# Performance work log

Hardware: AMD Instinct MI355X
Metric: run time of the kernel (lower is better)

The kernel has to match this reference:

```python
import jax, jax.numpy as jnp
import numpy as np

B, C, H, W, L = 2, 64, 48, 48, 48
GH, GW, GL = 24, 24, 24  # gating signal at half resolution


def setup_inputs() -> dict:
    key = jax.random.key(0)
    k = jax.random.split(key, 6)
    x = jax.random.normal(k[0], (B, C, H, W, L), dtype=jnp.float32)
    g = jax.random.normal(k[1], (B, C, GH, GW, GL), dtype=jnp.float32)
    s = 1.0 / np.sqrt(C)
    W1 = jax.random.normal(k[2], (C, C), dtype=jnp.float32) * s  # conv1 1x1x1 weight (out,in)
    b1 = jax.random.normal(k[3], (C,), dtype=jnp.float32) * 0.01
    W2 = jax.random.normal(k[4], (C, C), dtype=jnp.float32) * s  # conv2 1x1x1 weight
    b2 = jax.random.normal(k[5], (C,), dtype=jnp.float32) * 0.01
    return {"x": x, "g": g, "W1": W1, "b1": b1, "W2": W2, "b2": b2}


def _conv1x1(v, Wm, b):
    # 1x1x1 Conv3d == channel-mixing matmul
    return jnp.einsum('bchwl,oc->bohwl', v, Wm) + b[None, :, None, None, None]


def reference(x, g, W1, b1, W2, b2):
    theta_x = _conv1x1(x, W1, b1)                       # (B, C, H, W, L)
    theta_g = _conv1x1(g, W2, b2)                       # (B, C, GH, GW, GL)
    # F.upsample(mode='trilinear', align_corners=False) -> half-pixel trilinear resize
    theta_g = jax.image.resize(theta_g, (B, C, H, W, L), method='trilinear')

    # spatially-normalized elementwise gate
    theta_c = theta_x * theta_g
    theta_c = theta_c - jnp.min(theta_c)                # global min over whole tensor
    theta_c = theta_c / jnp.sum(theta_c, axis=(2, 3, 4), keepdims=True)
    p = theta_c * x

    # channel-channel attention per (b,h,w), contracting over L
    theta_c_d = jnp.einsum('bihwl,bjhwl->bhwij', theta_x, theta_g)  # (B,H,W,C,C)
    theta_c_d = theta_c_d - jnp.min(theta_c_d)
    theta_c_d = theta_c_d / jnp.sum(theta_c_d, axis=(1, 2, 3, 4), keepdims=True)
    d = jnp.einsum('bchwl,bhwcj->bjhwl', x, theta_c_d)  # (B, C, H, W, L)
    return (p, d)
```

## Files before the change

### kernel.cpp

```cpp
#include <hip/hip_runtime.h>

#define Bb 2
#define Cc 64
#define Hh 48
#define Ww 48
#define Ll 48
#define HWc (Hh*Ww)
#define HWL (HWc*Ll)
#define GHh 24
#define SG (GHh*GHh*GHh)
#define NBLK (Bb*HWc)
#define CNT1f 110592.0f
#define CNT2f 9437184.0f

__device__ __forceinline__ void interp1(int i, int& a, int& b, float& f){
  float src = i*0.5f - 0.25f;
  float fl = floorf(src);
  f = src - fl;
  int i0 = (int)fl;
  a = i0 < 0 ? 0 : i0;
  int i1 = i0 + 1;
  b = i1 > (GHh-1) ? (GHh-1) : i1;
}

__global__ __launch_bounds__(256) void conv_k(const float* __restrict__ in,
    const float* __restrict__ Wm, const float* __restrict__ bias,
    float* __restrict__ out, int S){
  __shared__ __align__(16) float Wl[64][68];
  __shared__ __align__(16) float xl[64][68];
  int t = threadIdx.x;
  int ntile = S >> 6;
  int b  = blockIdx.x / ntile;
  int s0 = (blockIdx.x % ntile) << 6;
  for (int q = t; q < 4096; q += 256){
    int o = q >> 6, c = q & 63;
    Wl[c][o] = Wm[q];
  }
  const float* inb = in + (size_t)b*Cc*S + s0;
  for (int q = t; q < 1024; q += 256){
    int c = q >> 4, v = (q & 15) << 2;
    float4 val = *(const float4*)(inb + (size_t)c*S + v);
    *(float4*)&xl[c][v] = val;
  }
  __syncthreads();
  int o0 = (t & 15) << 2, s1 = (t >> 4) << 2;
  float a00=0,a01=0,a02=0,a03=0,a10=0,a11=0,a12=0,a13=0;
  float a20=0,a21=0,a22=0,a23=0,a30=0,a31=0,a32=0,a33=0;
  #pragma unroll 8
  for (int c = 0; c < 64; ++c){
    float4 wv = *(const float4*)&Wl[c][o0];
    float4 xv = *(const float4*)&xl[c][s1];
    a00 += wv.x*xv.x; a01 += wv.x*xv.y; a02 += wv.x*xv.z; a03 += wv.x*xv.w;
    a10 += wv.y*xv.x; a11 += wv.y*xv.y; a12 += wv.y*xv.z; a13 += wv.y*xv.w;
    a20 += wv.z*xv.x; a21 += wv.z*xv.y; a22 += wv.z*xv.z; a23 += wv.z*xv.w;
    a30 += wv.w*xv.x; a31 += wv.w*xv.y; a32 += wv.w*xv.z; a33 += wv.w*xv.w;
  }
  float* ob = out + (size_t)b*Cc*S + s0 + s1;
  float b0 = bias[o0+0], b1v = bias[o0+1], b2v = bias[o0+2], b3 = bias[o0+3];
  { float4 r = make_float4(a00+b0,a01+b0,a02+b0,a03+b0); *(float4*)(ob + (size_t)(o0+0)*S) = r; }
  { float4 r = make_float4(a10+b1v,a11+b1v,a12+b1v,a13+b1v); *(float4*)(ob + (size_t)(o0+1)*S) = r; }
  { float4 r = make_float4(a20+b2v,a21+b2v,a22+b2v,a23+b2v); *(float4*)(ob + (size_t)(o0+2)*S) = r; }
  { float4 r = make_float4(a30+b3,a31+b3,a32+b3,a33+b3); *(float4*)(ob + (size_t)(o0+3)*S) = r; }
}

__global__ __launch_bounds__(256) void upsample_k(const float* __restrict__ tgh,
    float* __restrict__ tg){
  __shared__ float shm[2][24][25];
  int t = threadIdx.x;
  int bc = blockIdx.x / Hh;
  int h  = blockIdx.x % Hh;
  int ha, hb; float fh; interp1(h, ha, hb, fh);
  const float* src = tgh + (size_t)bc*SG;
  for (int q = t; q < 288; q += 256){
    int p = q / 144, rem = q % 144;
    int w_ = rem / 6, vl = (rem % 6) << 2;
    int hs = p ? hb : ha;
    float4 v = *(const float4*)(src + (size_t)hs*576 + w_*24 + vl);
    shm[p][w_][vl+0]=v.x; shm[p][w_][vl+1]=v.y; shm[p][w_][vl+2]=v.z; shm[p][w_][vl+3]=v.w;
  }
  __syncthreads();
  float* dst = tg + ((size_t)bc*Hh + h)*HWc;
  float omf = 1.f - fh;
  #pragma unroll
  for (int k = 0; k < 9; ++k){
    int idx = t + (k << 8);
    int w = idx / 48, l = idx % 48;
    int wa, wb; float fw; interp1(w, wa, wb, fw);
    int la, lb; float fl; interp1(l, la, lb, fl);
    float vaa = omf*shm[0][wa][la] + fh*shm[1][wa][la];
    float vab = omf*shm[0][wa][lb] + fh*shm[1][wa][lb];
    float vba = omf*shm[0][wb][la] + fh*shm[1][wb][la];
    float vbb = omf*shm[0][wb][lb] + fh*shm[1][wb][lb];
    float va = (1.f-fw)*vaa + fw*vba;
    float vb = (1.f-fw)*vab + fw*vbb;
    dst[idx] = (1.f-fl)*va + fl*vb;
  }
}

__global__ __launch_bounds__(256) void reduce_k(const float* __restrict__ tx,
    const float* __restrict__ tg, float* __restrict__ part_row,
    float* __restrict__ pm1, float* __restrict__ pm2, float* __restrict__ ps2){
  __shared__ __align__(16) float txt[48][68];
  __shared__ __align__(16) float tgt[48][68];
  __shared__ float red[512];
  __shared__ float sxg[48];
  int t = threadIdx.x;
  int bIdx = blockIdx.x;
  int b = bIdx / HWc, hw = bIdx % HWc;
  const float* txb = tx + ((size_t)b*Cc*HWc + hw)*Ll;
  const float* tgb = tg + ((size_t)b*Cc*HWc + hw)*Ll;
  for (int q = t; q < 768; q += 256){
    int c = q / 12, v = (q % 12) << 2;
    float4 a = *(const float4*)(txb + (size_t)c*HWL + v);
    txt[v+0][c]=a.x; txt[v+1][c]=a.y; txt[v+2][c]=a.z; txt[v+3][c]=a.w;
    float4 g = *(const float4*)(tgb + (size_t)c*HWL + v);
    tgt[v+0][c]=g.x; tgt[v+1][c]=g.y; tgt[v+2][c]=g.z; tgt[v+3][c]=g.w;
  }
  __syncthreads();
  int c = t & 63, lg = t >> 6;
  float psum = 0.f, pmin = 3.4e38f;
  #pragma unroll
  for (int li = 0; li < 12; ++li){
    int l = lg*12 + li;
    float prod = txt[l][c]*tgt[l][c];
    psum += prod;
    pmin = fminf(pmin, prod);
  }
  red[t] = psum;
  if (t < 48){
    float sx = 0.f, sg = 0.f;
    #pragma unroll 8
    for (int cc = 0; cc < 64; ++cc){ sx += txt[t][cc]; sg += tgt[t][cc]; }
    sxg[t] = sx*sg;
  }
  __syncthreads();
  if (t < 64) part_row[(size_t)bIdx*64 + t] = red[t]+red[t+64]+red[t+128]+red[t+192];
  int i0 = (t & 15) << 2, j0 = (t >> 4) << 2;
  float a00=0,a01=0,a02=0,a03=0,a10=0,a11=0,a12=0,a13=0;
  float a20=0,a21=0,a22=0,a23=0,a30=0,a31=0,a32=0,a33=0;
  #pragma unroll 4
  for (int l = 0; l < 48; ++l){
    float4 av = *(const float4*)&txt[l][i0];
    float4 bv = *(const float4*)&tgt[l][j0];
    a00 += av.x*bv.x; a01 += av.x*bv.y; a02 += av.x*bv.z; a03 += av.x*bv.w;
    a10 += av.y*bv.x; a11 += av.y*bv.y; a12 += av.y*bv.z; a13 += av.y*bv.w;
    a20 += av.z*bv.x; a21 += av.z*bv.y; a22 += av.z*bv.z; a23 += av.z*bv.w;
    a30 += av.w*bv.x; a31 += av.w*bv.y; a32 += av.w*bv.z; a33 += av.w*bv.w;
  }
  float amin = fminf(fminf(fminf(a00,a01),fminf(a02,a03)),
               fminf(fminf(fminf(a10,a11),fminf(a12,a13)),
               fminf(fminf(fminf(a20,a21),fminf(a22,a23)),
                     fminf(fminf(a30,a31),fminf(a32,a33)))));
  __syncthreads();
  red[t] = pmin; red[256+t] = amin;
  __syncthreads();
  if (t < 128){
    red[t] = fminf(red[t], red[t+128]);
    red[256+t] = fminf(red[256+t], red[256+t+128]);
  }
  __syncthreads();
  if (t < 64){
    float v1 = fminf(red[t], red[t+64]);
    float v2 = fminf(red[256+t], red[256+t+64]);
    #pragma unroll
    for (int off = 32; off; off >>= 1){
      v1 = fminf(v1, __shfl_down(v1, off));
      v2 = fminf(v2, __shfl_down(v2, off));
    }
    if (t == 0){
      pm1[bIdx] = v1; pm2[bIdx] = v2;
      float tot = 0.f;
      #pragma unroll
      for (int l = 0; l < 48; ++l) tot += sxg[l];
      ps2[bIdx] = tot;
    }
  }
}

__global__ __launch_bounds__(256) void reduce2_k(const float* __restrict__ part_row,
    const float* __restrict__ pm1, const float* __restrict__ pm2,
    const float* __restrict__ ps2, float* __restrict__ rowsum,
    float* __restrict__ gmin, float* __restrict__ s2v){
  __shared__ float red[512];
  int t = threadIdx.x, blk = blockIdx.x;
  if (blk < 128){
    int b = blk >> 6, c = blk & 63;
    const float* src = part_row + (size_t)b*HWc*64 + c;
    float s = 0.f;
    #pragma unroll
    for (int k = 0; k < 9; ++k){
      int i = t + (k << 8);
      s += src[(size_t)i*64];
    }
    red[t] = s; __syncthreads();
    for (int sgap = 128; sgap >= 64; sgap >>= 1){
      if (t < sgap) red[t] += red[t+sgap];
      __syncthreads();
    }
    if (t < 64){
      float v = red[t];
      #pragma unroll
      for (int off = 32; off; off >>= 1) v += __shfl_down(v, off);
      if (t == 0) rowsum[blk] = v;
    }
  } else if (blk == 128){
    float m1 = 3.4e38f, m2 = 3.4e38f;
    for (int i = t; i < NBLK; i += 256){ m1 = fminf(m1, pm1[i]); m2 = fminf(m2, pm2[i]); }
    red[t] = m1; red[256+t] = m2; __syncthreads();
    for (int s = 128; s >= 1; s >>= 1){
      if (t < s){ red[t] = fminf(red[t], red[t+s]); red[256+t] = fminf(red[256+t], red[256+t+s]); }
      __syncthreads();
    }
    if (t == 0){ gmin[0] = red[0]; gmin[1] = red[256]; }
  } else {
    float sa = 0.f, sb = 0.f;
    for (int i = t; i < HWc; i += 256){ sa += ps2[i]; sb += ps2[HWc + i]; }
    red[t] = sa; red[256+t] = sb; __syncthreads();
    for (int s = 128; s >= 1; s >>= 1){
      if (t < s){ red[t] += red[t+s]; red[256+t] += red[256+t+s]; }
      __syncthreads();
    }
    if (t == 0){ s2v[0] = red[0]; s2v[1] = red[256]; }
  }
}

__global__ __launch_bounds__(256) void final_k(const float* __restrict__ x,
    const float* __restrict__ tx, const float* __restrict__ tg,
    const float* __restrict__ gmin, const float* __restrict__ rowsum,
    const float* __restrict__ s2v, float* __restrict__ outp, float* __restrict__ outd){
  __shared__ __align__(16) float sh[6528 + 3328 + 48 + 64];
  float* txt = sh;
  float* tgt = sh + 3264;
  float* At  = sh;
  float* xs  = sh + 6528;
  float* Xs  = sh + 6528 + 3328;
  float* iv1 = Xs + 48;
  int t = threadIdx.x;
  int bIdx = blockIdx.x;
  int b = bIdx / HWc, hw = bIdx % HWc;
  size_t sbase = ((size_t)b*Cc*HWc + hw)*Ll;
  const float* txb = tx + sbase;
  const float* tgb = tg + sbase;
  const float* xb  = x  + sbase;
  for (int q = t; q < 768; q += 256){
    int c = q / 12, v = (q % 12) << 2;
    float4 a = *(const float4*)(txb + (size_t)c*HWL + v);
    txt[(v+0)*68+c]=a.x; txt[(v+1)*68+c]=a.y; txt[(v+2)*68+c]=a.z; txt[(v+3)*68+c]=a.w;
    float4 g = *(const float4*)(tgb + (size_t)c*HWL + v);
    tgt[(v+0)*68+c]=g.x; tgt[(v+1)*68+c]=g.y; tgt[(v+2)*68+c]=g.z; tgt[(v+3)*68+c]=g.w;
    float4 xv = *(const float4*)(xb + (size_t)c*HWL + v);
    *(float4*)&xs[c*52 + v] = xv;
  }
  __syncthreads();
  if (t < 48){
    float s = 0.f;
    #pragma unroll 8
    for (int cc = 0; cc < 64; ++cc) s += xs[cc*52 + t];
    Xs[t] = s;
  }
  float m1 = gmin[0], m2 = gmin[1];
  if (t < 64) iv1[t] = 1.f/(rowsum[b*64 + t] - m1*CNT1f);
  float invd2 = 1.f/(s2v[b] - m2*CNT2f);
  int i0 = (t & 15) << 2, j0 = (t >> 4) << 2;
  float a00=0,a01=0,a02=0,a03=0,a10=0,a11=0,a12=0,a13=0;
  float a20=0,a21=0,a22=0,a23=0,a30=0,a31=0,a32=0,a33=0;
  #pragma unroll 4
  for (int l = 0; l < 48; ++l){
    float4 av = *(const float4*)&txt[l*68 + i0];
    float4 bv = *(const float4*)&tgt[l*68 + j0];
    a00 += av.x*bv.x; a01 += av.x*bv.y; a02 += av.x*bv.z; a03 += av.x*bv.w;
    a10 += av.y*bv.x; a11 += av.y*bv.y; a12 += av.y*bv.z; a13 += av.y*bv.w;
    a20 += av.z*bv.x; a21 += av.z*bv.y; a22 += av.z*bv.z; a23 += av.z*bv.w;
    a30 += av.w*bv.x; a31 += av.w*bv.y; a32 += av.w*bv.z; a33 += av.w*bv.w;
  }
  __syncthreads();
  #pragma unroll
  for (int k = 0; k < 12; ++k){
    int e = t + (k << 8);
    int cc = e / 48, l = e % 48;
    float pv = (txt[l*68+cc]*tgt[l*68+cc] - m1)*iv1[cc]*xs[cc*52+l];
    outp[sbase + (size_t)cc*HWL + l] = pv;
  }
  __syncthreads();
  { float4 r = make_float4(a00,a01,a02,a03); *(float4*)&At[(i0+0)*68 + j0] = r; }
  { float4 r = make_float4(a10,a11,a12,a13); *(float4*)&At[(i0+1)*68 + j0] = r; }
  { float4 r = make_float4(a20,a21,a22,a23); *(float4*)&At[(i0+2)*68 + j0] = r; }
  { float4 r = make_float4(a30,a31,a32,a33); *(float4*)&At[(i0+3)*68 + j0] = r; }
  __syncthreads();
  if (t < 192){
    int jj = (t & 15) << 2, l0 = (t >> 4) << 2;
    float d00=0,d01=0,d02=0,d03=0,d10=0,d11=0,d12=0,d13=0;
    float d20=0,d21=0,d22=0,d23=0,d30=0,d31=0,d32=0,d33=0;
    #pragma unroll 4
    for (int cc = 0; cc < 64; ++cc){
      float4 av = *(const float4*)&At[cc*68 + jj];
      float4 xv = *(const float4*)&xs[cc*52 + l0];
      d00 += av.x*xv.x; d01 += av.x*xv.y; d02 += av.x*xv.z; d03 += av.x*xv.w;
      d10 += av.y*xv.x; d11 += av.y*xv.y; d12 += av.y*xv.z; d13 += av.y*xv.w;
      d20 += av.z*xv.x; d21 += av.z*xv.y; d22 += av.z*xv.z; d23 += av.z*xv.w;
      d30 += av.w*xv.x; d31 += av.w*xv.y; d32 += av.w*xv.z; d33 += av.w*xv.w;
    }
    float xs0 = m2*Xs[l0+0], xs1 = m2*Xs[l0+1], xs2 = m2*Xs[l0+2], xs3 = m2*Xs[l0+3];
    { float4 r = make_float4((d00-xs0)*invd2,(d01-xs1)*invd2,(d02-xs2)*invd2,(d03-xs3)*invd2);
      *(float4*)(outd + sbase + (size_t)(jj+0)*HWL + l0) = r; }
    { float4 r = make_float4((d10-xs0)*invd2,(d11-xs1)*invd2,(d12-xs2)*invd2,(d13-xs3)*invd2);
      *(float4*)(outd + sbase + (size_t)(jj+1)*HWL + l0) = r; }
    { float4 r = make_float4((d20-xs0)*invd2,(d21-xs1)*invd2,(d22-xs2)*invd2,(d23-xs3)*invd2);
      *(float4*)(outd + sbase + (size_t)(jj+2)*HWL + l0) = r; }
    { float4 r = make_float4((d30-xs0)*invd2,(d31-xs1)*invd2,(d32-xs2)*invd2,(d33-xs3)*invd2);
      *(float4*)(outd + sbase + (size_t)(jj+3)*HWL + l0) = r; }
  }
}

extern "C" void kernel_launch(void* const* d_in, const int* in_sizes, int n_in,
                              void* d_out, int out_size, void* d_ws, size_t ws_size,
                              hipStream_t stream){
  (void)in_sizes; (void)n_in; (void)out_size; (void)ws_size;
  const float* x  = (const float*)d_in[0];
  const float* g  = (const float*)d_in[1];
  const float* W1 = (const float*)d_in[2];
  const float* b1 = (const float*)d_in[3];
  const float* W2 = (const float*)d_in[4];
  const float* b2 = (const float*)d_in[5];
  float* outp = (float*)d_out;
  float* outd = outp + (size_t)Bb*Cc*HWL;
  float* ws   = (float*)d_ws;
  float* txw  = ws;
  float* tgw  = txw + (size_t)Bb*Cc*HWL;
  float* tghw = tgw + (size_t)Bb*Cc*HWL;
  float* part_row = tghw + (size_t)Bb*Cc*SG;
  float* pm1 = part_row + (size_t)NBLK*64;
  float* pm2 = pm1 + NBLK;
  float* ps2 = pm2 + NBLK;
  float* rowsum = ps2 + NBLK;
  float* gmin = rowsum + 128;
  float* s2v  = gmin + 2;

  hipLaunchKernelGGL(conv_k, dim3(Bb*(SG/64)), dim3(256), 0, stream, g, W2, b2, tghw, SG);
  hipLaunchKernelGGL(conv_k, dim3(Bb*(HWL/64)), dim3(256), 0, stream, x, W1, b1, txw, HWL);
  hipLaunchKernelGGL(upsample_k, dim3(Bb*Cc*Hh), dim3(256), 0, stream, tghw, tgw);
  hipLaunchKernelGGL(reduce_k, dim3(NBLK), dim3(256), 0, stream, txw, tgw, part_row, pm1, pm2, ps2);
  hipLaunchKernelGGL(reduce2_k, dim3(130), dim3(256), 0, stream, part_row, pm1, pm2, ps2, rowsum, gmin, s2v);
  hipLaunchKernelGGL(final_k, dim3(NBLK), dim3(256), 0, stream, x, txw, tgw, gmin, rowsum, s2v, outp, outd);
}
```

Baseline: 327.8 us.

## Cache per-position channel attention matrix from reduce pass and reuse in final kernel

The reduce kernel now writes its 64x64 tx·tg product per (b,h,w) to workspace when enough workspace is available. A new final kernel loads that matrix instead of recomputing it from tx and tg, folding the min shift into the load. This removes the second contraction over L but adds a large global write and read of the cached matrices. It falls back to the old path if the workspace is too small.

After: 360.2 us. 9.9% more time.

```diff
diff --git a/kernel.cpp b/kernel.cpp
--- a/kernel.cpp
+++ b/kernel.cpp
@@ -99,7 +99,8 @@
 
 __global__ __launch_bounds__(256) void reduce_k(const float* __restrict__ tx,
     const float* __restrict__ tg, float* __restrict__ part_row,
-    float* __restrict__ pm1, float* __restrict__ pm2, float* __restrict__ ps2){
+    float* __restrict__ pm1, float* __restrict__ pm2, float* __restrict__ ps2,
+    float* __restrict__ Atg){
   __shared__ __align__(16) float txt[48][68];
   __shared__ __align__(16) float tgt[48][68];
   __shared__ float red[512];
@@ -151,6 +152,13 @@
                fminf(fminf(fminf(a10,a11),fminf(a12,a13)),
                fminf(fminf(fminf(a20,a21),fminf(a22,a23)),
                      fminf(fminf(a30,a31),fminf(a32,a33)))));
+  if (Atg){
+    float* ab = Atg + (size_t)bIdx*4096 + (size_t)i0*64 + j0;
+    { float4 r = make_float4(a00,a01,a02,a03); *(float4*)(ab +   0) = r; }
+    { float4 r = make_float4(a10,a11,a12,a13); *(float4*)(ab +  64) = r; }
+    { float4 r = make_float4(a20,a21,a22,a23); *(float4*)(ab + 128) = r; }
+    { float4 r = make_float4(a30,a31,a32,a33); *(float4*)(ab + 192) = r; }
+  }
   __syncthreads();
   red[t] = pmin; red[256+t] = amin;
   __syncthreads();
@@ -221,6 +229,71 @@
       __syncthreads();
     }
     if (t == 0){ s2v[0] = red[0]; s2v[1] = red[256]; }
+  }
+}
+
+__global__ __launch_bounds__(256) void final2_k(const float* __restrict__ x,
+    const float* __restrict__ tx, const float* __restrict__ tg,
+    const float* __restrict__ Atg, const float* __restrict__ gmin,
+    const float* __restrict__ rowsum, const float* __restrict__ s2v,
+    float* __restrict__ outp, float* __restrict__ outd){
+  __shared__ __align__(16) float xs[64][52];
+  __shared__ __align__(16) float AtL[64][68];
+  __shared__ float iv1[64];
+  int t = threadIdx.x;
+  int bIdx = blockIdx.x;
+  int b = bIdx / HWc, hw = bIdx % HWc;
+  size_t sbase = ((size_t)b*Cc*HWc + hw)*Ll;
+  const float* xb = x + sbase;
+  float m1 = gmin[0], m2 = gmin[1];
+  for (int q = t; q < 768; q += 256){
+    int c = q / 12, v = (q % 12) << 2;
+    *(float4*)&xs[c][v] = *(const float4*)(xb + (size_t)c*HWL + v);
+  }
+  const float* ab = Atg + (size_t)bIdx*4096;
+  for (int q = t; q < 1024; q += 256){
+    float4 a = *(const float4*)(ab + (q << 2));
+    int i = q >> 4, j = (q & 15) << 2;
+    a.x -= m2; a.y -= m2; a.z -= m2; a.w -= m2;
+    *(float4*)&AtL[i][j] = a;
+  }
+  if (t < 64) iv1[t] = 1.f/(rowsum[b*64 + t] - m1*CNT1f);
+  float invd2 = 1.f/(s2v[b] - m2*CNT2f);
+  __syncthreads();
+  #pragma unroll
+  for (int k = 0; k < 3; ++k){
+    int f = t + (k << 8);
+    int c = f / 12, l4 = (f % 12) << 2;
+    size_t off = sbase + (size_t)c*HWL + l4;
+    float4 a = *(const float4*)(tx + off);
+    float4 g = *(const float4*)(tg + off);
+    float4 xv = *(const float4*)&xs[c][l4];
+    float s = iv1[c];
+    float4 r = make_float4((a.x*g.x - m1)*s*xv.x, (a.y*g.y - m1)*s*xv.y,
+                           (a.z*g.z - m1)*s*xv.z, (a.w*g.w - m1)*s*xv.w);
+    *(float4*)(outp + off) = r;
+  }
+  if (t < 192){
+    int jj = (t & 15) << 2, l0 = (t >> 4) << 2;
+    float d00=0,d01=0,d02=0,d03=0,d10=0,d11=0,d12=0,d13=0;
+    float d20=0,d21=0,d22=0,d23=0,d30=0,d31=0,d32=0,d33=0;
+    #pragma unroll 4
+    for (int cc = 0; cc < 64; ++cc){
+      float4 av = *(const float4*)&AtL[cc][jj];
+      float4 xv = *(const float4*)&xs[cc][l0];
+      d00 += av.x*xv.x; d01 += av.x*xv.y; d02 += av.x*xv.z; d03 += av.x*xv.w;
+      d10 += av.y*xv.x; d11 += av.y*xv.y; d12 += av.y*xv.z; d13 += av.y*xv.w;
+      d20 += av.z*xv.x; d21 += av.z*xv.y; d22 += av.z*xv.z; d23 += av.z*xv.w;
+      d30 += av.w*xv.x; d31 += av.w*xv.y; d32 += av.w*xv.z; d33 += av.w*xv.w;
+    }
+    { float4 r = make_float4(d00*invd2,d01*invd2,d02*invd2,d03*invd2);
+      *(float4*)(outd + sbase + (size_t)(jj+0)*HWL + l0) = r; }
+    { float4 r = make_float4(d10*invd2,d11*invd2,d12*invd2,d13*invd2);
+      *(float4*)(outd + sbase + (size_t)(jj+1)*HWL + l0) = r; }
+    { float4 r = make_float4(d20*invd2,d21*invd2,d22*invd2,d23*invd2);
+      *(float4*)(outd + sbase + (size_t)(jj+2)*HWL + l0) = r; }
+    { float4 r = make_float4(d30*invd2,d31*invd2,d32*invd2,d33*invd2);
+      *(float4*)(outd + sbase + (size_t)(jj+3)*HWL + l0) = r; }
   }
 }
 
@@ -315,7 +388,7 @@
 extern "C" void kernel_launch(void* const* d_in, const int* in_sizes, int n_in,
                               void* d_out, int out_size, void* d_ws, size_t ws_size,
                               hipStream_t stream){
-  (void)in_sizes; (void)n_in; (void)out_size; (void)ws_size;
+  (void)in_sizes; (void)n_in; (void)out_size;
   const float* x  = (const float*)d_in[0];
   const float* g  = (const float*)d_in[1];
   const float* W1 = (const float*)d_in[2];
@@ -335,11 +408,24 @@
   float* rowsum = ps2 + NBLK;
   float* gmin = rowsum + 128;
   float* s2v  = gmin + 2;
+  float* Atg  = s2v + 2;
+
+  size_t base_floats = (size_t)Bb*Cc*HWL*2 + (size_t)Bb*Cc*SG + (size_t)NBLK*64
+                     + 3*(size_t)NBLK + 128 + 4;
+  size_t need_bytes = (base_floats + (size_t)NBLK*4096) * sizeof(float);
+  int useAt = (ws_size >= need_bytes);
 
   hipLaunchKernelGGL(conv_k, dim3(Bb*(SG/64)), dim3(256), 0, stream, g, W2, b2, tghw, SG);
   hipLaunchKernelGGL(conv_k, dim3(Bb*(HWL/64)), dim3(256), 0, stream, x, W1, b1, txw, HWL);
   hipLaunchKernelGGL(upsample_k, dim3(Bb*Cc*Hh), dim3(256), 0, stream, tghw, tgw);
-  hipLaunchKernelGGL(reduce_k, dim3(NBLK), dim3(256), 0, stream, txw, tgw, part_row, pm1, pm2, ps2);
-  hipLaunchKernelGGL(reduce2_k, dim3(130), dim3(256), 0, stream, part_row, pm1, pm2, ps2, rowsum, gmin, s2v);
-  hipLaunchKernelGGL(final_k, dim3(NBLK), dim3(256), 0, stream, x, txw, tgw, gmin, rowsum, s2v, outp, outd);
-}
+  hipLaunchKernelGGL(reduce_k, dim3(NBLK), dim3(256), 0, stream, txw, tgw, part_row,
+                     pm1, pm2, ps2, useAt ? Atg : (float*)nullptr);
+  hipLaunchKernelGGL(reduce2_k, dim3(130), dim3(256), 0, stream, part_row, pm1, pm2, ps2,
+                     rowsum, gmin, s2v);
+  if (useAt)
+    hipLaunchKernelGGL(final2_k, dim3(NBLK), dim3(256), 0, stream, x, txw, tgw, Atg,
+                       gmin, rowsum, s2v, outp, outd);
+  else
+    hipLaunchKernelGGL(final_k, dim3(NBLK), dim3(256), 0, stream, x, txw, tgw,
+                       gmin, rowsum, s2v, outp, outd);
+}
```

## Fuse trilinear upsample into reduce kernel and store gate per site contiguously

Applied to the files above, without the earlier changes.

Removes the separate upsample kernel. reduce_k now interpolates the half-resolution gate directly for each (b,h,w) site and writes it to a per-site contiguous buffer, which final_k then reads with contiguous float4 loads. Both kernels switch their shared tiles to a channel-major layout with stride 52, and the min/normalisation of the attention matrix is folded in before the second matmul. The gate is still written once, so the main saving is one launch, the strided gate reads and the transposed shared stores. In exchange reduce_k does redundant scattered gathers from the low-resolution tensor.

Measured after the change: 330.9 us. About the same (+0.9%).

```diff
diff --git a/kernel.cpp b/kernel.cpp
--- a/kernel.cpp
+++ b/kernel.cpp
@@ -63,105 +63,126 @@
   { float4 r = make_float4(a30+b3,a31+b3,a32+b3,a33+b3); *(float4*)(ob + (size_t)(o0+3)*S) = r; }
 }
 
-__global__ __launch_bounds__(256) void upsample_k(const float* __restrict__ tgh,
-    float* __restrict__ tg){
-  __shared__ float shm[2][24][25];
-  int t = threadIdx.x;
-  int bc = blockIdx.x / Hh;
-  int h  = blockIdx.x % Hh;
-  int ha, hb; float fh; interp1(h, ha, hb, fh);
-  const float* src = tgh + (size_t)bc*SG;
-  for (int q = t; q < 288; q += 256){
-    int p = q / 144, rem = q % 144;
-    int w_ = rem / 6, vl = (rem % 6) << 2;
-    int hs = p ? hb : ha;
-    float4 v = *(const float4*)(src + (size_t)hs*576 + w_*24 + vl);
-    shm[p][w_][vl+0]=v.x; shm[p][w_][vl+1]=v.y; shm[p][w_][vl+2]=v.z; shm[p][w_][vl+3]=v.w;
-  }
-  __syncthreads();
-  float* dst = tg + ((size_t)bc*Hh + h)*HWc;
-  float omf = 1.f - fh;
-  #pragma unroll
-  for (int k = 0; k < 9; ++k){
-    int idx = t + (k << 8);
-    int w = idx / 48, l = idx % 48;
-    int wa, wb; float fw; interp1(w, wa, wb, fw);
-    int la, lb; float fl; interp1(l, la, lb, fl);
-    float vaa = omf*shm[0][wa][la] + fh*shm[1][wa][la];
-    float vab = omf*shm[0][wa][lb] + fh*shm[1][wa][lb];
-    float vba = omf*shm[0][wb][la] + fh*shm[1][wb][la];
-    float vbb = omf*shm[0][wb][lb] + fh*shm[1][wb][lb];
-    float va = (1.f-fw)*vaa + fw*vba;
-    float vb = (1.f-fw)*vab + fw*vbb;
-    dst[idx] = (1.f-fl)*va + fl*vb;
-  }
-}
-
 __global__ __launch_bounds__(256) void reduce_k(const float* __restrict__ tx,
-    const float* __restrict__ tg, float* __restrict__ part_row,
-    float* __restrict__ pm1, float* __restrict__ pm2, float* __restrict__ ps2){
-  __shared__ __align__(16) float txt[48][68];
-  __shared__ __align__(16) float tgt[48][68];
+    const float* __restrict__ tgh, float* __restrict__ tgsite,
+    float* __restrict__ part_row, float* __restrict__ pm1,
+    float* __restrict__ pm2, float* __restrict__ ps2){
+  __shared__ __align__(16) float txt[64*52];
+  __shared__ __align__(16) float tgt[64*52];
+  __shared__ float Msh[64*25];
   __shared__ float red[512];
   __shared__ float sxg[48];
   int t = threadIdx.x;
   int bIdx = blockIdx.x;
   int b = bIdx / HWc, hw = bIdx % HWc;
+  int h = hw / Ww, w = hw % Ww;
+  int ha, hb; float fh; interp1(h, ha, hb, fh);
+  int wa, wb; float fw; interp1(w, wa, wb, fw);
+  float omh = 1.f - fh, omw = 1.f - fw;
   const float* txb = tx + ((size_t)b*Cc*HWc + hw)*Ll;
-  const float* tgb = tg + ((size_t)b*Cc*HWc + hw)*Ll;
-  for (int q = t; q < 768; q += 256){
+  #pragma unroll
+  for (int k = 0; k < 3; ++k){
+    int q = t + (k << 8);
     int c = q / 12, v = (q % 12) << 2;
-    float4 a = *(const float4*)(txb + (size_t)c*HWL + v);
-    txt[v+0][c]=a.x; txt[v+1][c]=a.y; txt[v+2][c]=a.z; txt[v+3][c]=a.w;
-    float4 g = *(const float4*)(tgb + (size_t)c*HWL + v);
-    tgt[v+0][c]=g.x; tgt[v+1][c]=g.y; tgt[v+2][c]=g.z; tgt[v+3][c]=g.w;
-  }
-  __syncthreads();
-  int c = t & 63, lg = t >> 6;
+    *(float4*)&txt[c*52+v] = *(const float4*)(txb + (size_t)c*HWL + v);
+  }
+  const float* gb = tgh + (size_t)b*Cc*SG;
+  #pragma unroll
+  for (int k = 0; k < 6; ++k){
+    int q = t + (k << 8);
+    int c = q / 24, j = q % 24;
+    const float* gc = gb + (size_t)c*SG;
+    float vaa = gc[ha*576 + wa*24 + j];
+    float vba = gc[hb*576 + wa*24 + j];
+    float vab = gc[ha*576 + wb*24 + j];
+    float vbb = gc[hb*576 + wb*24 + j];
+    float mwa = omh*vaa + fh*vba;
+    float mwb = omh*vab + fh*vbb;
+    Msh[c*25 + j] = omw*mwa + fw*mwb;
+  }
+  __syncthreads();
+  float* tgs = tgsite + (size_t)bIdx*3072;
+  #pragma unroll
+  for (int k = 0; k < 3; ++k){
+    int q = t + (k << 8);
+    int c = q / 12, l4 = (q % 12) << 2;
+    float4 r;
+    float* rp = &r.x;
+    #pragma unroll
+    for (int i = 0; i < 4; ++i){
+      int l = l4 + i;
+      int la, lb; float fl; interp1(l, la, lb, fl);
+      rp[i] = (1.f-fl)*Msh[c*25+la] + fl*Msh[c*25+lb];
+    }
+    *(float4*)&tgt[c*52+l4] = r;
+    *(float4*)(tgs + c*48 + l4) = r;
+  }
+  __syncthreads();
+  int c = t & 63, lq = t >> 6;
   float psum = 0.f, pmin = 3.4e38f;
   #pragma unroll
-  for (int li = 0; li < 12; ++li){
-    int l = lg*12 + li;
-    float prod = txt[l][c]*tgt[l][c];
-    psum += prod;
-    pmin = fminf(pmin, prod);
+  for (int m = 0; m < 3; ++m){
+    int l4 = (lq << 2) + (m << 4);
+    float4 a = *(const float4*)&txt[c*52+l4];
+    float4 g = *(const float4*)&tgt[c*52+l4];
+    float p0 = a.x*g.x, p1 = a.y*g.y, p2 = a.z*g.z, p3 = a.w*g.w;
+    psum += p0+p1+p2+p3;
+    pmin = fminf(pmin, fminf(fminf(p0,p1), fminf(p2,p3)));
   }
   red[t] = psum;
   if (t < 48){
     float sx = 0.f, sg = 0.f;
     #pragma unroll 8
-    for (int cc = 0; cc < 64; ++cc){ sx += txt[t][cc]; sg += tgt[t][cc]; }
+    for (int cc = 0; cc < 64; ++cc){ sx += txt[cc*52+t]; sg += tgt[cc*52+t]; }
     sxg[t] = sx*sg;
   }
-  __syncthreads();
-  if (t < 64) part_row[(size_t)bIdx*64 + t] = red[t]+red[t+64]+red[t+128]+red[t+192];
   int i0 = (t & 15) << 2, j0 = (t >> 4) << 2;
   float a00=0,a01=0,a02=0,a03=0,a10=0,a11=0,a12=0,a13=0;
   float a20=0,a21=0,a22=0,a23=0,a30=0,a31=0,a32=0,a33=0;
   #pragma unroll 4
-  for (int l = 0; l < 48; ++l){
-    float4 av = *(const float4*)&txt[l][i0];
-    float4 bv = *(const float4*)&tgt[l][j0];
-    a00 += av.x*bv.x; a01 += av.x*bv.y; a02 += av.x*bv.z; a03 += av.x*bv.w;
-    a10 += av.y*bv.x; a11 += av.y*bv.y; a12 += av.y*bv.z; a13 += av.y*bv.w;
-    a20 += av.z*bv.x; a21 += av.z*bv.y; a22 += av.z*bv.z; a23 += av.z*bv.w;
-    a30 += av.w*bv.x; a31 += av.w*bv.y; a32 += av.w*bv.z; a33 += av.w*bv.w;
+  for (int l0 = 0; l0 < 48; l0 += 4){
+    float4 x0 = *(const float4*)&txt[(i0+0)*52 + l0];
+    float4 x1 = *(const float4*)&txt[(i0+1)*52 + l0];
+    float4 x2 = *(const float4*)&txt[(i0+2)*52 + l0];
+    float4 x3 = *(const float4*)&txt[(i0+3)*52 + l0];
+    float4 g0 = *(const float4*)&tgt[(j0+0)*52 + l0];
+    float4 g1 = *(const float4*)&tgt[(j0+1)*52 + l0];
+    float4 g2 = *(const float4*)&tgt[(j0+2)*52 + l0];
+    float4 g3 = *(const float4*)&tgt[(j0+3)*52 + l0];
+    a00 += x0.x*g0.x + x0.y*g0.y + x0.z*g0.z + x0.w*g0.w;
+    a01 += x0.x*g1.x + x0.y*g1.y + x0.z*g1.z + x0.w*g1.w;
+    a02 += x0.x*g2.x + x0.y*g2.y + x0.z*g2.z + x0.w*g2.w;
+    a03 += x0.x*g3.x + x0.y*g3.y + x0.z*g3.z + x0.w*g3.w;
+    a10 += x1.x*g0.x + x1.y*g0.y + x1.z*g0.z + x1.w*g0.w;
+    a11 += x1.x*g1.x + x1.y*g1.y + x1.z*g1.z + x1.w*g1.w;
+    a12 += x1.x*g2.x + x1.y*g2.y + x1.z*g2.z + x1.w*g2.w;
+    a13 += x1.x*g3.x + x1.y*g3.y + x1.z*g3.z + x1.w*g3.w;
+    a20 += x2.x*g0.x + x2.y*g0.y + x2.z*g0.z + x2.w*g0.w;
+    a21 += x2.x*g1.x + x2.y*g1.y + x2.z*g1.z + x2.w*g1.w;
+    a22 += x2.x*g2.x + x2.y*g2.y + x2.z*g2.z + x2.w*g2.w;
+    a23 += x2.x*g3.x + x2.y*g3.y + x2.z*g3.z + x2.w*g3.w;
+    a30 += x3.x*g0.x + x3.y*g0.y + x3.z*g0.z + x3.w*g0.w;
+    a31 += x3.x*g1.x + x3.y*g1.y + x3.z*g1.z + x3.w*g1.w;
+    a32 += x3.x*g2.x + x3.y*g2.y + x3.z*g2.z + x3.w*g2.w;
+    a33 += x3.x*g3.x + x3.y*g3.y + x3.z*g3.z + x3.w*g3.w;
   }
   float amin = fminf(fminf(fminf(a00,a01),fminf(a02,a03)),
                fminf(fminf(fminf(a10,a11),fminf(a12,a13)),
                fminf(fminf(fminf(a20,a21),fminf(a22,a23)),
                      fminf(fminf(a30,a31),fminf(a32,a33)))));
   __syncthreads();
+  if (t < 64) part_row[(size_t)bIdx*64 + t] = red[t]+red[t+64]+red[t+128]+red[t+192];
+  __syncthreads();
   red[t] = pmin; red[256+t] = amin;
   __syncthreads();
   if (t < 128){
     red[t] = fminf(red[t], red[t+128]);
-    red[256+t] = fminf(red[256+t], red[256+t+128]);
+    red[256+t] = fminf(red[256+t], red[384+t]);
   }
   __syncthreads();
   if (t < 64){
     float v1 = fminf(red[t], red[t+64]);
-    float v2 = fminf(red[256+t], red[256+t+64]);
+    float v2 = fminf(red[256+t], red[320+t]);
     #pragma unroll
     for (int off = 32; off; off >>= 1){
       v1 = fminf(v1, __shfl_down(v1, off));
@@ -225,67 +246,84 @@
 }
 
 __global__ __launch_bounds__(256) void final_k(const float* __restrict__ x,
-    const float* __restrict__ tx, const float* __restrict__ tg,
+    const float* __restrict__ tx, const float* __restrict__ tgsite,
     const float* __restrict__ gmin, const float* __restrict__ rowsum,
     const float* __restrict__ s2v, float* __restrict__ outp, float* __restrict__ outd){
-  __shared__ __align__(16) float sh[6528 + 3328 + 48 + 64];
-  float* txt = sh;
-  float* tgt = sh + 3264;
-  float* At  = sh;
-  float* xs  = sh + 6528;
-  float* Xs  = sh + 6528 + 3328;
-  float* iv1 = Xs + 48;
+  __shared__ __align__(16) float txt[64*52];
+  __shared__ __align__(16) float tgt[64*52];
+  __shared__ __align__(16) float xs[64*52];
+  __shared__ float iv1[64];
   int t = threadIdx.x;
   int bIdx = blockIdx.x;
   int b = bIdx / HWc, hw = bIdx % HWc;
   size_t sbase = ((size_t)b*Cc*HWc + hw)*Ll;
   const float* txb = tx + sbase;
-  const float* tgb = tg + sbase;
   const float* xb  = x  + sbase;
-  for (int q = t; q < 768; q += 256){
+  const float* tgs = tgsite + (size_t)bIdx*3072;
+  float m1 = gmin[0], m2 = gmin[1];
+  #pragma unroll
+  for (int k = 0; k < 3; ++k){
+    int q = t + (k << 8);
     int c = q / 12, v = (q % 12) << 2;
-    float4 a = *(const float4*)(txb + (size_t)c*HWL + v);
-    txt[(v+0)*68+c]=a.x; txt[(v+1)*68+c]=a.y; txt[(v+2)*68+c]=a.z; txt[(v+3)*68+c]=a.w;
-    float4 g = *(const float4*)(tgb + (size_t)c*HWL + v);
-    tgt[(v+0)*68+c]=g.x; tgt[(v+1)*68+c]=g.y; tgt[(v+2)*68+c]=g.z; tgt[(v+3)*68+c]=g.w;
-    float4 xv = *(const float4*)(xb + (size_t)c*HWL + v);
-    *(float4*)&xs[c*52 + v] = xv;
-  }
-  __syncthreads();
-  if (t < 48){
-    float s = 0.f;
-    #pragma unroll 8
-    for (int cc = 0; cc < 64; ++cc) s += xs[cc*52 + t];
-    Xs[t] = s;
-  }
-  float m1 = gmin[0], m2 = gmin[1];
+    *(float4*)&txt[c*52+v] = *(const float4*)(txb + (size_t)c*HWL + v);
+    *(float4*)&xs [c*52+v] = *(const float4*)(xb  + (size_t)c*HWL + v);
+    *(float4*)&tgt[c*52+v] = *(const float4*)(tgs + (q << 2));
+  }
   if (t < 64) iv1[t] = 1.f/(rowsum[b*64 + t] - m1*CNT1f);
   float invd2 = 1.f/(s2v[b] - m2*CNT2f);
+  __syncthreads();
   int i0 = (t & 15) << 2, j0 = (t >> 4) << 2;
   float a00=0,a01=0,a02=0,a03=0,a10=0,a11=0,a12=0,a13=0;
   float a20=0,a21=0,a22=0,a23=0,a30=0,a31=0,a32=0,a33=0;
   #pragma unroll 4
-  for (int l = 0; l < 48; ++l){
-    float4 av = *(const float4*)&txt[l*68 + i0];
-    float4 bv = *(const float4*)&tgt[l*68 + j0];
-    a00 += av.x*bv.x; a01 += av.x*bv.y; a02 += av.x*bv.z; a03 += av.x*bv.w;
-    a10 += av.y*bv.x; a11 += av.y*bv.y; a12 += av.y*bv.z; a13 += av.y*bv.w;
-    a20 += av.z*bv.x; a21 += av.z*bv.y; a22 += av.z*bv.z; a23 += av.z*bv.w;
-    a30 += av.w*bv.x; a31 += av.w*bv.y; a32 += av.w*bv.z; a33 += av.w*bv.w;
-  }
-  __syncthreads();
-  #pragma unroll
-  for (int k = 0; k < 12; ++k){
-    int e = t + (k << 8);
-    int cc = e / 48, l = e % 48;
-    float pv = (txt[l*68+cc]*tgt[l*68+cc] - m1)*iv1[cc]*xs[cc*52+l];
-    outp[sbase + (size_t)cc*HWL + l] = pv;
-  }
-  __syncthreads();
-  { float4 r = make_float4(a00,a01,a02,a03); *(float4*)&At[(i0+0)*68 + j0] = r; }
-  { float4 r = make_float4(a10,a11,a12,a13); *(float4*)&At[(i0+1)*68 + j0] = r; }
-  { float4 r = make_float4(a20,a21,a22,a23); *(float4*)&At[(i0+2)*68 + j0] = r; }
-  { float4 r = make_float4(a30,a31,a32,a33); *(float4*)&At[(i0+3)*68 + j0] = r; }
+  for (int l0 = 0; l0 < 48; l0 += 4){
+    float4 x0 = *(const float4*)&txt[(i0+0)*52 + l0];
+    float4 x1 = *(const float4*)&txt[(i0+1)*52 + l0];
+    float4 x2 = *(const float4*)&txt[(i0+2)*52 + l0];
+    float4 x3 = *(const float4*)&txt[(i0+3)*52 + l0];
+    float4 g0 = *(const float4*)&tgt[(j0+0)*52 + l0];
+    float4 g1 = *(const float4*)&tgt[(j0+1)*52 + l0];
+    float4 g2 = *(const float4*)&tgt[(j0+2)*52 + l0];
+    float4 g3 = *(const float4*)&tgt[(j0+3)*52 + l0];
+    a00 += x0.x*g0.x + x0.y*g0.y + x0.z*g0.z + x0.w*g0.w;
+    a01 += x0.x*g1.x + x0.y*g1.y + x0.z*g1.z + x0.w*g1.w;
+    a02 += x0.x*g2.x + x0.y*g2.y + x0.z*g2.z + x0.w*g2.w;
+    a03 += x0.x*g3.x + x0.y*g3.y + x0.z*g3.z + x0.w*g3.w;
+    a10 += x1.x*g0.x + x1.y*g0.y + x1.z*g0.z + x1.w*g0.w;
+    a11 += x1.x*g1.x + x1.y*g1.y + x1.z*g1.z + x1.w*g1.w;
+    a12 += x1.x*g2.x + x1.y*g2.y + x1.z*g2.z + x1.w*g2.w;
+    a13 += x1.x*g3.x + x1.y*g3.y + x1.z*g3.z + x1.w*g3.w;
+    a20 += x2.x*g0.x + x2.y*g0.y + x2.z*g0.z + x2.w*g0.w;
+    a21 += x2.x*g1.x + x2.y*g1.y + x2.z*g1.z + x2.w*g1.w;
+    a22 += x2.x*g2.x + x2.y*g2.y + x2.z*g2.z + x2.w*g2.w;
+    a23 += x2.x*g3.x + x2.y*g3.y + x2.z*g3.z + x2.w*g3.w;
+    a30 += x3.x*g0.x + x3.y*g0.y + x3.z*g0.z + x3.w*g0.w;
+    a31 += x3.x*g1.x + x3.y*g1.y + x3.z*g1.z + x3.w*g1.w;
+    a32 += x3.x*g2.x + x3.y*g2.y + x3.z*g2.z + x3.w*g2.w;
+    a33 += x3.x*g3.x + x3.y*g3.y + x3.z*g3.z + x3.w*g3.w;
+  }
+  #pragma unroll
+  for (int k = 0; k < 3; ++k){
+    int q = t + (k << 8);
+    int c = q / 12, l4 = (q % 12) << 2;
+    float4 a = *(const float4*)&txt[c*52+l4];
+    float4 g = *(const float4*)&tgt[c*52+l4];
+    float4 xv = *(const float4*)&xs[c*52+l4];
+    float s = iv1[c];
+    float4 r = make_float4((a.x*g.x - m1)*s*xv.x, (a.y*g.y - m1)*s*xv.y,
+                           (a.z*g.z - m1)*s*xv.z, (a.w*g.w - m1)*s*xv.w);
+    *(float4*)(outp + sbase + (size_t)c*HWL + l4) = r;
+  }
+  __syncthreads();
+  float* At = txt;
+  { float4 r = make_float4((a00-m2)*invd2,(a01-m2)*invd2,(a02-m2)*invd2,(a03-m2)*invd2);
+    *(float4*)&At[(i0+0)*52 + j0] = r; }
+  { float4 r = make_float4((a10-m2)*invd2,(a11-m2)*invd2,(a12-m2)*invd2,(a13-m2)*invd2);
+    *(float4*)&At[(i0+1)*52 + j0] = r; }
+  { float4 r = make_float4((a20-m2)*invd2,(a21-m2)*invd2,(a22-m2)*invd2,(a23-m2)*invd2);
+    *(float4*)&At[(i0+2)*52 + j0] = r; }
+  { float4 r = make_float4((a30-m2)*invd2,(a31-m2)*invd2,(a32-m2)*invd2,(a33-m2)*invd2);
+    *(float4*)&At[(i0+3)*52 + j0] = r; }
   __syncthreads();
   if (t < 192){
     int jj = (t & 15) << 2, l0 = (t >> 4) << 2;
@@ -293,21 +331,20 @@
     float d20=0,d21=0,d22=0,d23=0,d30=0,d31=0,d32=0,d33=0;
     #pragma unroll 4
     for (int cc = 0; cc < 64; ++cc){
-      float4 av = *(const float4*)&At[cc*68 + jj];
+      float4 av = *(const float4*)&At[cc*52 + jj];
       float4 xv = *(const float4*)&xs[cc*52 + l0];
       d00 += av.x*xv.x; d01 += av.x*xv.y; d02 += av.x*xv.z; d03 += av.x*xv.w;
       d10 += av.y*xv.x; d11 += av.y*xv.y; d12 += av.y*xv.z; d13 += av.y*xv.w;
       d20 += av.z*xv.x; d21 += av.z*xv.y; d22 += av.z*xv.z; d23 += av.z*xv.w;
       d30 += av.w*xv.x; d31 += av.w*xv.y; d32 += av.w*xv.z; d33 += av.w*xv.w;
     }
-    float xs0 = m2*Xs[l0+0], xs1 = m2*Xs[l0+1], xs2 = m2*Xs[l0+2], xs3 = m2*Xs[l0+3];
-    { float4 r = make_float4((d00-xs0)*invd2,(d01-xs1)*invd2,(d02-xs2)*invd2,(d03-xs3)*invd2);
+    { float4 r = make_float4(d00,d01,d02,d03);
       *(float4*)(outd + sbase + (size_t)(jj+0)*HWL + l0) = r; }
-    { float4 r = make_float4((d10-xs0)*invd2,(d11-xs1)*invd2,(d12-xs2)*invd2,(d13-xs3)*invd2);
+    { float4 r = make_float4(d10,d11,d12,d13);
       *(float4*)(outd + sbase + (size_t)(jj+1)*HWL + l0) = r; }
-    { float4 r = make_float4((d20-xs0)*invd2,(d21-xs1)*invd2,(d22-xs2)*invd2,(d23-xs3)*invd2);
+    { float4 r = make_float4(d20,d21,d22,d23);
       *(float4*)(outd + sbase + (size_t)(jj+2)*HWL + l0) = r; }
-    { float4 r = make_float4((d30-xs0)*invd2,(d31-xs1)*invd2,(d32-xs2)*invd2,(d33-xs3)*invd2);
+    { float4 r = make_float4(d30,d31,d32,d33);
       *(float4*)(outd + sbase + (size_t)(jj+3)*HWL + l0) = r; }
   }
 }
@@ -325,10 +362,10 @@
   float* outp = (float*)d_out;
   float* outd = outp + (size_t)Bb*Cc*HWL;
   float* ws   = (float*)d_ws;
-  float* txw  = ws;
-  float* tgw  = txw + (size_t)Bb*Cc*HWL;
-  float* tghw = tgw + (size_t)Bb*Cc*HWL;
-  float* part_row = tghw + (size_t)Bb*Cc*SG;
+  float* txw    = ws;
+  float* tghw   = txw + (size_t)Bb*Cc*HWL;
+  float* tgsite = tghw + (size_t)Bb*Cc*SG;
+  float* part_row = tgsite + (size_t)Bb*Cc*HWL;
   float* pm1 = part_row + (size_t)NBLK*64;
   float* pm2 = pm1 + NBLK;
   float* ps2 = pm2 + NBLK;
@@ -338,8 +375,10 @@
 
   hipLaunchKernelGGL(conv_k, dim3(Bb*(SG/64)), dim3(256), 0, stream, g, W2, b2, tghw, SG);
   hipLaunchKernelGGL(conv_k, dim3(Bb*(HWL/64)), dim3(256), 0, stream, x, W1, b1, txw, HWL);
-  hipLaunchKernelGGL(upsample_k, dim3(Bb*Cc*Hh), dim3(256), 0, stream, tghw, tgw);
-  hipLaunchKernelGGL(reduce_k, dim3(NBLK), dim3(256), 0, stream, txw, tgw, part_row, pm1, pm2, ps2);
-  hipLaunchKernelGGL(reduce2_k, dim3(130), dim3(256), 0, stream, part_row, pm1, pm2, ps2, rowsum, gmin, s2v);
-  hipLaunchKernelGGL(final_k, dim3(NBLK), dim3(256), 0, stream, x, txw, tgw, gmin, rowsum, s2v, outp, outd);
-}
+  hipLaunchKernelGGL(reduce_k, dim3(NBLK), dim3(256), 0, stream, txw, tghw, tgsite,
+                     part_row, pm1, pm2, ps2);
+  hipLaunchKernelGGL(reduce2_k, dim3(130), dim3(256), 0, stream, part_row, pm1, pm2, ps2,
+                     rowsum, gmin, s2v);
+  hipLaunchKernelGGL(final_k, dim3(NBLK), dim3(256), 0, stream, x, txw, tgsite,
+                     gmin, rowsum, s2v, outp, outd);
+}
```
